# Optimization experiments

Measured on AMD Instinct MI355X. Metric: run time of the kernel, lower is better.

Reference implementation:

```python
import jax, jax.numpy as jnp
import numpy as np

QWEN_H = 2048
SNN_H = 512


def setup_inputs() -> dict:
    key = jax.random.key(0)
    k0, k1, k2, k3, k4 = jax.random.split(key, 5)
    hidden_states = jax.random.normal(k0, (4, 2048, QWEN_H), dtype=jnp.float32)
    # nn.Linear weights stored as [out, in]
    w_down = jax.random.normal(k1, (SNN_H, QWEN_H), dtype=jnp.float32) / np.sqrt(QWEN_H)
    w_up = jax.random.normal(k2, (QWEN_H, SNN_H), dtype=jnp.float32) / np.sqrt(SNN_H)
    w1 = jax.random.normal(k3, (SNN_H, SNN_H), dtype=jnp.float32) / np.sqrt(SNN_H)
    w2 = jax.random.normal(k4, (SNN_H, SNN_H), dtype=jnp.float32) / np.sqrt(SNN_H)
    residual_scale = jnp.float32(0.1)
    return {"hidden_states": hidden_states, "w_down": w_down, "w_up": w_up,
            "w1": w1, "w2": w2, "residual_scale": residual_scale}


def reference(hidden_states, w_down, w_up, w1, w2, residual_scale):
    # Faithful math of SNNMiddleLayer.forward. The spike pulse encode ->
    # SpikeFP32Linear (fp32 accumulation) -> pulse decode path is a lossless
    # FP32 spike encoding of an ordinary bias-free linear layer, so the
    # per-timestep loop computes exactly out_t = w2 @ (w1 @ proj_down(x_t)),
    # which we express as fused batched GEMMs over all timesteps.
    residual = hidden_states
    x = jnp.einsum('bsq,hq->bsh', hidden_states, w_down)   # proj_down
    h = jnp.einsum('bsh,oh->bso', x, w1)                   # snn_linear1
    o = jnp.einsum('bso,po->bsp', h, w2)                   # snn_linear2
    out = jnp.einsum('bsp,qp->bsq', o, w_up)               # proj_up
    return residual + residual_scale * out
```

## Files before the change

### kernel.cpp

```cpp
#include <hip/hip_runtime.h>
#include <hip/hip_bf16.h>
#include <stdint.h>

using bf16 = __hip_bfloat16;
typedef __attribute__((ext_vector_type(8))) short bf16x8;
typedef __attribute__((ext_vector_type(4))) float f32x4;

__device__ __forceinline__ void async_load16(const void* g, void* l) {
    __builtin_amdgcn_global_load_lds(
        (__attribute__((address_space(1))) const void*)g,
        (__attribute__((address_space(3))) void*)l,
        16, 0, 0);
}

__device__ __forceinline__ void cvt_block_2048(const float* __restrict__ src,
                                               bf16* __restrict__ dst, int relblk) {
    int i = (relblk * 256 + (int)threadIdx.x) * 8;
    float4 f0 = *(const float4*)(src + i);
    float4 f1 = *(const float4*)(src + i + 4);
    union { bf16 h[8]; uint4 u; } o;
    o.h[0] = __float2bfloat16(f0.x); o.h[1] = __float2bfloat16(f0.y);
    o.h[2] = __float2bfloat16(f0.z); o.h[3] = __float2bfloat16(f0.w);
    o.h[4] = __float2bfloat16(f1.x); o.h[5] = __float2bfloat16(f1.y);
    o.h[6] = __float2bfloat16(f1.z); o.h[7] = __float2bfloat16(f1.w);
    *(uint4*)(dst + i) = o.u;
}

__global__ __launch_bounds__(256) void prep_w(
    const float* __restrict__ w1, bf16* __restrict__ w1b,
    const float* __restrict__ wup, bf16* __restrict__ wub,
    const float* __restrict__ wd, bf16* __restrict__ wdt,
    const float* __restrict__ w2, bf16* __restrict__ w2t) {
    __shared__ bf16 sh[32][33];
    int b = blockIdx.x;
    if (b < 128)       { cvt_block_2048(w1, w1b, b); return; }
    if (b < 640)       { cvt_block_2048(wup, wub, b - 128); return; }
    const float* src; bf16* dst; int R, C, tile, ntx;
    if (b < 1664) { src = wd; dst = wdt; R = 512; C = 2048; tile = b - 640; ntx = 64; }
    else          { src = w2; dst = w2t; R = 512; C = 512;  tile = b - 1664; ntx = 16; }
    const int bx = (tile % ntx) * 32, by = (tile / ntx) * 32;
    const int lx = threadIdx.x & 31;
    const int ly4 = ((int)threadIdx.x >> 5) * 4;
#pragma unroll
    for (int r = 0; r < 4; ++r)
        sh[ly4 + r][lx] = __float2bfloat16(src[(size_t)(by + ly4 + r) * C + bx + lx]);
    __syncthreads();
#pragma unroll
    for (int r = 0; r < 4; ++r)
        dst[(size_t)(bx + ly4 + r) * R + by + lx] = sh[lx][ly4 + r];
}

template<int BN, int BK>
__device__ __forceinline__ void stage_tiles(
    const bf16* __restrict__ A, const bf16* __restrict__ B,
    size_t bm, size_t bn, int K, int k0,
    bf16* __restrict__ As, bf16* __restrict__ Bs, int wave, int lane)
{
    if constexpr (BK == 64) {
        const int srow = lane >> 3;
        const int scol = (lane & 7) ^ srow;
        constexpr int NCH = (128 + BN) / 8;
#pragma unroll
        for (int c = 0; c < NCH / 4; ++c) {
            const int cc = wave + c * 4;
            if (cc < 16) {
                const int rb = cc * 8;
                async_load16(A + (bm + rb + srow) * (size_t)K + k0 + scol * 8,
                             &As[rb * 64]);
            } else {
                const int rb = (cc - 16) * 8;
                async_load16(B + (bn + rb + srow) * (size_t)K + k0 + scol * 8,
                             &Bs[rb * 64]);
            }
        }
    } else {
        const int sr = lane >> 2;
        const int sc = (lane & 3) ^ ((sr >> 1) & 3);
        constexpr int NCH = (128 + BN) / 16;
#pragma unroll
        for (int c = 0; c < NCH / 4; ++c) {
            const int cc = wave + c * 4;
            if (cc < 8) {
                const int rb = cc * 16;
                async_load16(A + (bm + rb + sr) * (size_t)K + k0 + sc * 8,
                             &As[rb * 32]);
            } else {
                const int rb = (cc - 8) * 16;
                async_load16(B + (bn + rb + sr) * (size_t)K + k0 + sc * 8,
                             &Bs[rb * 32]);
            }
        }
    }
}

template<int BN, int EPI, int BK, int KT>
__device__ __forceinline__ void gemm_core(
    const bf16* __restrict__ A, const bf16* __restrict__ B,
    bf16* __restrict__ Cb, float* __restrict__ Cf,
    const float* __restrict__ Res, const float* __restrict__ sp,
    int N, int K, int bxi, int byi, bf16* smem)
{
    constexpr int BM = 128;
    constexpr int NJ = BN / 32;
    constexpr int BUF = (BM + BN) * BK;
    static_assert(BN == 64 || BN == 128, "BN");
    static_assert(BK == 32 || BK == 64, "BK");
    static_assert(EPI == 0 || (KT > 0 && KT / BK == 16), "EPI=1 needs 16 unrolled K-iters");

    const int tid  = threadIdx.x;
    const int wave = tid >> 6;
    const int lane = tid & 63;
    const int wm = wave >> 1, wn = wave & 1;
    const size_t bm = (size_t)bxi * BM;
    const size_t bn = (size_t)byi * BN;

    f32x4 acc[4][NJ];
#pragma unroll
    for (int i = 0; i < 4; ++i)
#pragma unroll
        for (int j = 0; j < NJ; ++j)
            acc[i][j] = (f32x4){0.f, 0.f, 0.f, 0.f};

    float4 res_pre[EPI ? 16 : 1];
    const int r16 = lane >> 3;
    const int cbb = (lane & 7) * 4;

    auto compute_tile = [&](const bf16* Ap, const bf16* Bp) {
        if constexpr (BK == 64) {
#pragma unroll
            for (int kk = 0; kk < 2; ++kk) {
                const int c8 = kk * 4 + (lane >> 4);
                bf16x8 af[4], bfr[NJ];
#pragma unroll
                for (int i = 0; i < 4; ++i) {
                    const int r = wm * 64 + i * 16 + (lane & 15);
                    af[i] = *(const bf16x8*)&Ap[(size_t)(r * 8 + (c8 ^ (r & 7))) * 8];
                }
#pragma unroll
                for (int j = 0; j < NJ; ++j) {
                    const int r = wn * (BN / 2) + j * 16 + (lane & 15);
                    bfr[j] = *(const bf16x8*)&Bp[(size_t)(r * 8 + (c8 ^ (r & 7))) * 8];
                }
#pragma unroll
                for (int i = 0; i < 4; ++i)
#pragma unroll
                    for (int j = 0; j < NJ; ++j)
                        acc[i][j] = __builtin_amdgcn_mfma_f32_16x16x32_bf16(af[i], bfr[j], acc[i][j], 0, 0, 0);
            }
        } else {
            const int c4 = lane >> 4;
            bf16x8 af[4], bfr[NJ];
#pragma unroll
            for (int i = 0; i < 4; ++i) {
                const int r = wm * 64 + i * 16 + (lane & 15);
                af[i] = *(const bf16x8*)&Ap[(size_t)(r * 4 + (c4 ^ ((r >> 1) & 3))) * 8];
            }
#pragma unroll
            for (int j = 0; j < NJ; ++j) {
                const int r = wn * (BN / 2) + j * 16 + (lane & 15);
                bfr[j] = *(const bf16x8*)&Bp[(size_t)(r * 4 + (c4 ^ ((r >> 1) & 3))) * 8];
            }
#pragma unroll
            for (int i = 0; i < 4; ++i)
#pragma unroll
                for (int j = 0; j < NJ; ++j)
                    acc[i][j] = __builtin_amdgcn_mfma_f32_16x16x32_bf16(af[i], bfr[j], acc[i][j], 0, 0, 0);
        }
    };

    stage_tiles<BN, BK>(A, B, bm, bn, K, 0, smem, smem + BM * BK, wave, lane);
    __syncthreads();

    if constexpr (KT > 0) {
#pragma unroll
        for (int it = 0; it < KT / BK; ++it) {
            const int k0 = it * BK;
            const int cur = it & 1;
            if (k0 + BK < KT) {
                bf16* nb = smem + (cur ^ 1) * BUF;
                stage_tiles<BN, BK>(A, B, bm, bn, KT, k0 + BK, nb, nb + BM * BK, wave, lane);
            }
            if constexpr (EPI) {
                const int i = it >> 2, rh = (it >> 1) & 1, ch = it & 1;
                size_t row = bm + wm * 64 + i * 16 + rh * 8 + r16;
                size_t col = bn + wn * 64 + cbb + ch * 32;
                res_pre[it] = *(const float4*)&Res[row * (size_t)N + col];
            }
            const bf16* Ap = smem + cur * BUF;
            compute_tile(Ap, Ap + BM * BK);
            __syncthreads();
        }
    } else {
        int cur = 0;
        for (int k0 = 0; k0 < K; k0 += BK) {
            if (k0 + BK < K) {
                bf16* nb = smem + (cur ^ 1) * BUF;
                stage_tiles<BN, BK>(A, B, bm, bn, K, k0 + BK, nb, nb + BM * BK, wave, lane);
            }
            const bf16* Ap = smem + cur * BUF;
            compute_tile(Ap, Ap + BM * BK);
            __syncthreads();
            cur ^= 1;
        }
    }

    const int col_l = lane & 15;
    const int row_l = (lane >> 4) * 4;
    if (EPI == 0) {
#pragma unroll
        for (int i = 0; i < 4; ++i)
#pragma unroll
            for (int j = 0; j < NJ; ++j)
#pragma unroll
                for (int r = 0; r < 4; ++r) {
                    size_t row = bm + wm * 64 + i * 16 + row_l + r;
                    size_t col = bn + wn * (BN / 2) + j * 16 + col_l;
                    Cb[row * (size_t)N + col] = __float2bfloat16(acc[i][j][r]);
                }
    } else {
        const float s = *sp;
        float* lds_f = (float*)smem + wave * (16 * 68);
#pragma unroll
        for (int i = 0; i < 4; ++i) {
#pragma unroll
            for (int j = 0; j < NJ; ++j)
#pragma unroll
                for (int r = 0; r < 4; ++r)
                    lds_f[(row_l + r) * 68 + j * 16 + col_l] = acc[i][j][r];
            __syncthreads();
#pragma unroll
            for (int rh = 0; rh < 2; ++rh)
#pragma unroll
                for (int ch = 0; ch < 2; ++ch) {
                    const int rr = rh * 8 + r16;
                    const int cb = cbb + ch * 32;
                    float4 v = *(float4*)&lds_f[rr * 68 + cb];
                    size_t row = bm + wm * 64 + i * 16 + rr;
                    size_t col = bn + wn * 64 + cb;
                    size_t idx = row * (size_t)N + col;
                    float4 rv = res_pre[i * 4 + rh * 2 + ch];
                    float4 o;
                    o.x = rv.x + s * v.x; o.y = rv.y + s * v.y;
                    o.z = rv.z + s * v.z; o.w = rv.w + s * v.w;
                    *(float4*)&Cf[idx] = o;
                }
            __syncthreads();
        }
    }
}

template<int BN, int EPI, int BK, int KT>
__global__ __launch_bounds__(256) void gemm_bf16(
    const bf16* __restrict__ A, const bf16* __restrict__ B,
    bf16* __restrict__ Cb, float* __restrict__ Cf,
    const float* __restrict__ Res, const float* __restrict__ sp, int N, int K) {
    __shared__ __align__(16) bf16 smem[(128 + BN) * BK * 2];
    const int nx = gridDim.x;
    const int flat = blockIdx.y * nx + blockIdx.x;
    const int chunk = (nx * gridDim.y) >> 3;
    const int swz = (flat & 7) * chunk + (flat >> 3);
    gemm_core<BN, EPI, BK, KT>(A, B, Cb, Cf, Res, sp, N, K,
                               swz / nx, swz % nx, smem);
}

__global__ __launch_bounds__(256) void ru_cvt(
    const bf16* __restrict__ A0, const bf16* __restrict__ B0, bf16* __restrict__ C0,
    const bf16* __restrict__ A1, const bf16* __restrict__ B1, bf16* __restrict__ C1,
    const float* __restrict__ hs, bf16* __restrict__ hsb) {
    __shared__ __align__(16) bf16 smem[(128 + 64) * 64 * 2];
    int b = blockIdx.x;
    if (b < 128)
        gemm_core<64, 0, 64, 0>(A0, B0, C0, nullptr, nullptr, nullptr, 2048, 512,
                                b / 32, b % 32, smem);
    else if (b < 256) {
        int bb = b - 128;
        gemm_core<64, 0, 64, 0>(A1, B1, C1, nullptr, nullptr, nullptr, 512, 512,
                                bb / 8, bb % 8, smem);
    } else
        cvt_block_2048(hs, hsb, b - 256);
}

extern "C" void kernel_launch(void* const* d_in, const int* in_sizes, int n_in,
                              void* d_out, int out_size, void* d_ws, size_t ws_size,
                              hipStream_t stream) {
    const float* hs     = (const float*)d_in[0];
    const float* w_down = (const float*)d_in[1];
    const float* w_up   = (const float*)d_in[2];
    const float* w1     = (const float*)d_in[3];
    const float* w2     = (const float*)d_in[4];
    const float* rs     = (const float*)d_in[5];

    char* ws = (char*)d_ws;
    bf16* hs_b  = (bf16*)(ws + 0);
    bf16* x_b   = (bf16*)(ws + 33554432);
    bf16* w1_b  = (bf16*)(ws + 41943040);
    bf16* wu_b  = (bf16*)(ws + 42467328);
    bf16* wdt_b = (bf16*)(ws + 44564480);
    bf16* w2t_b = (bf16*)(ws + 46661632);
    bf16* Rm    = (bf16*)(ws + 47185920);
    bf16* Um    = (bf16*)(ws + 49283072);

    prep_w<<<dim3(1920), dim3(256), 0, stream>>>(w1, w1_b, w_up, wu_b, w_down, wdt_b, w2, w2t_b);
    ru_cvt<<<dim3(256 + 8192), dim3(256), 0, stream>>>(w1_b, wdt_b, Rm, wu_b, w2t_b, Um, hs, hs_b);
    gemm_bf16<64, 0, 64, 0><<<dim3(8, 64), dim3(256), 0, stream>>>(hs_b, Rm, x_b, nullptr,
                                                                   nullptr, nullptr, 512, 2048);
    gemm_bf16<128, 1, 32, 512><<<dim3(16, 64), dim3(256), 0, stream>>>(x_b, Um, nullptr, (float*)d_out,
                                                                       hs, rs, 2048, 512);
}
```

Before: 185.2 us.

## Use 8-wave 128x128 GEMM blocks with 64x32 wave tiles and BK=64

Restructures the GEMM core so each wave owns a 64x32 output tile, so 512-thread blocks cover 128x128 tiles. The down-projection GEMM moves from 128x64 to 128x128 tiles with a smaller grid. The up-projection epilogue GEMM switches from BK=32 to BK=64, which doubles shared memory per block. The epilogue uses per-wave LDS regions, so the block-wide barriers around the residual write are dropped. The aim is more reuse per block and fewer barriers, at the cost of more LDS and registers per block and therefore fewer resident blocks.

```diff
diff --git a/kernel.cpp b/kernel.cpp
--- a/kernel.cpp
+++ b/kernel.cpp
@@ -50,50 +50,31 @@
         dst[(size_t)(bx + ly4 + r) * R + by + lx] = sh[lx][ly4 + r];
 }
 
-template<int BN, int BK>
+template<int BN, int NW>
 __device__ __forceinline__ void stage_tiles(
     const bf16* __restrict__ A, const bf16* __restrict__ B,
     size_t bm, size_t bn, int K, int k0,
     bf16* __restrict__ As, bf16* __restrict__ Bs, int wave, int lane)
 {
-    if constexpr (BK == 64) {
-        const int srow = lane >> 3;
-        const int scol = (lane & 7) ^ srow;
-        constexpr int NCH = (128 + BN) / 8;
-#pragma unroll
-        for (int c = 0; c < NCH / 4; ++c) {
-            const int cc = wave + c * 4;
-            if (cc < 16) {
-                const int rb = cc * 8;
-                async_load16(A + (bm + rb + srow) * (size_t)K + k0 + scol * 8,
-                             &As[rb * 64]);
-            } else {
-                const int rb = (cc - 16) * 8;
-                async_load16(B + (bn + rb + srow) * (size_t)K + k0 + scol * 8,
-                             &Bs[rb * 64]);
-            }
-        }
-    } else {
-        const int sr = lane >> 2;
-        const int sc = (lane & 3) ^ ((sr >> 1) & 3);
-        constexpr int NCH = (128 + BN) / 16;
-#pragma unroll
-        for (int c = 0; c < NCH / 4; ++c) {
-            const int cc = wave + c * 4;
-            if (cc < 8) {
-                const int rb = cc * 16;
-                async_load16(A + (bm + rb + sr) * (size_t)K + k0 + sc * 8,
-                             &As[rb * 32]);
-            } else {
-                const int rb = (cc - 8) * 16;
-                async_load16(B + (bn + rb + sr) * (size_t)K + k0 + sc * 8,
-                             &Bs[rb * 32]);
-            }
+    const int srow = lane >> 3;
+    const int scol = (lane & 7) ^ srow;
+    constexpr int NCH = (128 + BN) / 8;
+#pragma unroll
+    for (int c = 0; c < NCH / NW; ++c) {
+        const int cc = wave + c * NW;
+        if (cc < 16) {
+            const int rb = cc * 8;
+            async_load16(A + (bm + rb + srow) * (size_t)K + k0 + scol * 8,
+                         &As[rb * 64]);
+        } else {
+            const int rb = (cc - 16) * 8;
+            async_load16(B + (bn + rb + srow) * (size_t)K + k0 + scol * 8,
+                         &Bs[rb * 64]);
         }
     }
 }
 
-template<int BN, int EPI, int BK, int KT>
+template<int BN, int EPI, int KT, int NW>
 __device__ __forceinline__ void gemm_core(
     const bf16* __restrict__ A, const bf16* __restrict__ B,
     bf16* __restrict__ Cb, float* __restrict__ Cf,
@@ -101,16 +82,18 @@
     int N, int K, int bxi, int byi, bf16* smem)
 {
     constexpr int BM = 128;
-    constexpr int NJ = BN / 32;
+    constexpr int BK = 64;
+    constexpr int WN = NW / 2;
+    constexpr int NJ = 2;
     constexpr int BUF = (BM + BN) * BK;
-    static_assert(BN == 64 || BN == 128, "BN");
-    static_assert(BK == 32 || BK == 64, "BK");
-    static_assert(EPI == 0 || (KT > 0 && KT / BK == 16), "EPI=1 needs 16 unrolled K-iters");
+    static_assert(BN == WN * 32, "wave tile is 64x32");
+    static_assert(NW == 4 || NW == 8, "NW");
+    static_assert(EPI == 0 || (NW == 8 && KT == 512), "EPI path: 8 waves, KT=512");
 
     const int tid  = threadIdx.x;
     const int wave = tid >> 6;
     const int lane = tid & 63;
-    const int wm = wave >> 1, wn = wave & 1;
+    const int wm = wave / WN, wn = wave % WN;
     const size_t bm = (size_t)bxi * BM;
     const size_t bn = (size_t)byi * BN;
 
@@ -121,44 +104,24 @@
         for (int j = 0; j < NJ; ++j)
             acc[i][j] = (f32x4){0.f, 0.f, 0.f, 0.f};
 
-    float4 res_pre[EPI ? 16 : 1];
+    float4 res_pre[EPI ? 8 : 1];
     const int r16 = lane >> 3;
     const int cbb = (lane & 7) * 4;
 
     auto compute_tile = [&](const bf16* Ap, const bf16* Bp) {
-        if constexpr (BK == 64) {
-#pragma unroll
-            for (int kk = 0; kk < 2; ++kk) {
-                const int c8 = kk * 4 + (lane >> 4);
-                bf16x8 af[4], bfr[NJ];
-#pragma unroll
-                for (int i = 0; i < 4; ++i) {
-                    const int r = wm * 64 + i * 16 + (lane & 15);
-                    af[i] = *(const bf16x8*)&Ap[(size_t)(r * 8 + (c8 ^ (r & 7))) * 8];
-                }
-#pragma unroll
-                for (int j = 0; j < NJ; ++j) {
-                    const int r = wn * (BN / 2) + j * 16 + (lane & 15);
-                    bfr[j] = *(const bf16x8*)&Bp[(size_t)(r * 8 + (c8 ^ (r & 7))) * 8];
-                }
-#pragma unroll
-                for (int i = 0; i < 4; ++i)
-#pragma unroll
-                    for (int j = 0; j < NJ; ++j)
-                        acc[i][j] = __builtin_amdgcn_mfma_f32_16x16x32_bf16(af[i], bfr[j], acc[i][j], 0, 0, 0);
-            }
-        } else {
-            const int c4 = lane >> 4;
+#pragma unroll
+        for (int kk = 0; kk < 2; ++kk) {
+            const int c8 = kk * 4 + (lane >> 4);
             bf16x8 af[4], bfr[NJ];
 #pragma unroll
             for (int i = 0; i < 4; ++i) {
                 const int r = wm * 64 + i * 16 + (lane & 15);
-                af[i] = *(const bf16x8*)&Ap[(size_t)(r * 4 + (c4 ^ ((r >> 1) & 3))) * 8];
+                af[i] = *(const bf16x8*)&Ap[(size_t)(r * 8 + (c8 ^ (r & 7))) * 8];
             }
 #pragma unroll
             for (int j = 0; j < NJ; ++j) {
-                const int r = wn * (BN / 2) + j * 16 + (lane & 15);
-                bfr[j] = *(const bf16x8*)&Bp[(size_t)(r * 4 + (c4 ^ ((r >> 1) & 3))) * 8];
+                const int r = wn * 32 + j * 16 + (lane & 15);
+                bfr[j] = *(const bf16x8*)&Bp[(size_t)(r * 8 + (c8 ^ (r & 7))) * 8];
             }
 #pragma unroll
             for (int i = 0; i < 4; ++i)
@@ -168,22 +131,21 @@
         }
     };
 
-    stage_tiles<BN, BK>(A, B, bm, bn, K, 0, smem, smem + BM * BK, wave, lane);
+    stage_tiles<BN, NW>(A, B, bm, bn, K, 0, smem, smem + BM * BK, wave, lane);
     __syncthreads();
 
     if constexpr (KT > 0) {
 #pragma unroll
         for (int it = 0; it < KT / BK; ++it) {
-            const int k0 = it * BK;
             const int cur = it & 1;
-            if (k0 + BK < KT) {
+            if (it + 1 < KT / BK) {
                 bf16* nb = smem + (cur ^ 1) * BUF;
-                stage_tiles<BN, BK>(A, B, bm, bn, KT, k0 + BK, nb, nb + BM * BK, wave, lane);
+                stage_tiles<BN, NW>(A, B, bm, bn, KT, (it + 1) * BK, nb, nb + BM * BK, wave, lane);
             }
             if constexpr (EPI) {
-                const int i = it >> 2, rh = (it >> 1) & 1, ch = it & 1;
+                const int i = it >> 1, rh = it & 1;
                 size_t row = bm + wm * 64 + i * 16 + rh * 8 + r16;
-                size_t col = bn + wn * 64 + cbb + ch * 32;
+                size_t col = bn + wn * 32 + cbb;
                 res_pre[it] = *(const float4*)&Res[row * (size_t)N + col];
             }
             const bf16* Ap = smem + cur * BUF;
@@ -195,7 +157,7 @@
         for (int k0 = 0; k0 < K; k0 += BK) {
             if (k0 + BK < K) {
                 bf16* nb = smem + (cur ^ 1) * BUF;
-                stage_tiles<BN, BK>(A, B, bm, bn, K, k0 + BK, nb, nb + BM * BK, wave, lane);
+                stage_tiles<BN, NW>(A, B, bm, bn, K, k0 + BK, nb, nb + BM * BK, wave, lane);
             }
             const bf16* Ap = smem + cur * BUF;
             compute_tile(Ap, Ap + BM * BK);
@@ -214,52 +176,47 @@
 #pragma unroll
                 for (int r = 0; r < 4; ++r) {
                     size_t row = bm + wm * 64 + i * 16 + row_l + r;
-                    size_t col = bn + wn * (BN / 2) + j * 16 + col_l;
+                    size_t col = bn + wn * 32 + j * 16 + col_l;
                     Cb[row * (size_t)N + col] = __float2bfloat16(acc[i][j][r]);
                 }
     } else {
         const float s = *sp;
-        float* lds_f = (float*)smem + wave * (16 * 68);
+        float* lds_f = (float*)smem + wave * (16 * 36);
 #pragma unroll
         for (int i = 0; i < 4; ++i) {
 #pragma unroll
             for (int j = 0; j < NJ; ++j)
 #pragma unroll
                 for (int r = 0; r < 4; ++r)
-                    lds_f[(row_l + r) * 68 + j * 16 + col_l] = acc[i][j][r];
-            __syncthreads();
-#pragma unroll
-            for (int rh = 0; rh < 2; ++rh)
-#pragma unroll
-                for (int ch = 0; ch < 2; ++ch) {
-                    const int rr = rh * 8 + r16;
-                    const int cb = cbb + ch * 32;
-                    float4 v = *(float4*)&lds_f[rr * 68 + cb];
-                    size_t row = bm + wm * 64 + i * 16 + rr;
-                    size_t col = bn + wn * 64 + cb;
-                    size_t idx = row * (size_t)N + col;
-                    float4 rv = res_pre[i * 4 + rh * 2 + ch];
-                    float4 o;
-                    o.x = rv.x + s * v.x; o.y = rv.y + s * v.y;
-                    o.z = rv.z + s * v.z; o.w = rv.w + s * v.w;
-                    *(float4*)&Cf[idx] = o;
-                }
-            __syncthreads();
+                    lds_f[(row_l + r) * 36 + j * 16 + col_l] = acc[i][j][r];
+#pragma unroll
+            for (int rh = 0; rh < 2; ++rh) {
+                const int rr = rh * 8 + r16;
+                float4 v = *(float4*)&lds_f[rr * 36 + cbb];
+                size_t row = bm + wm * 64 + i * 16 + rr;
+                size_t col = bn + wn * 32 + cbb;
+                size_t idx = row * (size_t)N + col;
+                float4 rv = res_pre[i * 2 + rh];
+                float4 o;
+                o.x = rv.x + s * v.x; o.y = rv.y + s * v.y;
+                o.z = rv.z + s * v.z; o.w = rv.w + s * v.w;
+                *(float4*)&Cf[idx] = o;
+            }
         }
     }
 }
 
-template<int BN, int EPI, int BK, int KT>
-__global__ __launch_bounds__(256) void gemm_bf16(
+template<int BN, int EPI, int KT, int NW>
+__global__ __launch_bounds__(NW * 64) void gemm_bf16(
     const bf16* __restrict__ A, const bf16* __restrict__ B,
     bf16* __restrict__ Cb, float* __restrict__ Cf,
     const float* __restrict__ Res, const float* __restrict__ sp, int N, int K) {
-    __shared__ __align__(16) bf16 smem[(128 + BN) * BK * 2];
+    __shared__ __align__(16) bf16 smem[(128 + BN) * 64 * 2];
     const int nx = gridDim.x;
     const int flat = blockIdx.y * nx + blockIdx.x;
     const int chunk = (nx * gridDim.y) >> 3;
     const int swz = (flat & 7) * chunk + (flat >> 3);
-    gemm_core<BN, EPI, BK, KT>(A, B, Cb, Cf, Res, sp, N, K,
+    gemm_core<BN, EPI, KT, NW>(A, B, Cb, Cf, Res, sp, N, K,
                                swz / nx, swz % nx, smem);
 }
 
@@ -270,12 +227,12 @@
     __shared__ __align__(16) bf16 smem[(128 + 64) * 64 * 2];
     int b = blockIdx.x;
     if (b < 128)
-        gemm_core<64, 0, 64, 0>(A0, B0, C0, nullptr, nullptr, nullptr, 2048, 512,
-                                b / 32, b % 32, smem);
+        gemm_core<64, 0, 0, 4>(A0, B0, C0, nullptr, nullptr, nullptr, 2048, 512,
+                               b / 32, b % 32, smem);
     else if (b < 256) {
         int bb = b - 128;
-        gemm_core<64, 0, 64, 0>(A1, B1, C1, nullptr, nullptr, nullptr, 512, 512,
-                                bb / 8, bb % 8, smem);
+        gemm_core<64, 0, 0, 4>(A1, B1, C1, nullptr, nullptr, nullptr, 512, 512,
+                               bb / 8, bb % 8, smem);
     } else
         cvt_block_2048(hs, hsb, b - 256);
 }
@@ -302,8 +259,8 @@
 
     prep_w<<<dim3(1920), dim3(256), 0, stream>>>(w1, w1_b, w_up, wu_b, w_down, wdt_b, w2, w2t_b);
     ru_cvt<<<dim3(256 + 8192), dim3(256), 0, stream>>>(w1_b, wdt_b, Rm, wu_b, w2t_b, Um, hs, hs_b);
-    gemm_bf16<64, 0, 64, 0><<<dim3(8, 64), dim3(256), 0, stream>>>(hs_b, Rm, x_b, nullptr,
+    gemm_bf16<128, 0, 0, 8><<<dim3(4, 64), dim3(512), 0, stream>>>(hs_b, Rm, x_b, nullptr,
                                                                    nullptr, nullptr, 512, 2048);
-    gemm_bf16<128, 1, 32, 512><<<dim3(16, 64), dim3(256), 0, stream>>>(x_b, Um, nullptr, (float*)d_out,
-                                                                       hs, rs, 2048, 512);
-}
+    gemm_bf16<128, 1, 512, 8><<<dim3(16, 64), dim3(512), 0, stream>>>(x_b, Um, nullptr, (float*)d_out,
+                                                                      hs, rs, 2048, 512);
+}
```

Result: no change. 182.6 us (-1.4%).
